# Kernel tuning notes

Measured on AMD Instinct MI355X. Metric: run time of the kernel, lower is better.

Reference implementation:

```python
import jax, jax.numpy as jnp
import numpy as np

L = 4        # transformer layers
C = 128      # width
CIN = 2      # obs channels
BS = 9       # boardsize
S = BS * BS  # attention sequence length (81)
EPS = 1e-5


def setup_inputs() -> dict:
    key = jax.random.key(0)
    ks = jax.random.split(key, 6)

    def w(k, shape, scale):
        return jax.random.normal(k, shape, dtype=jnp.float32) * scale

    return {
        "x": jax.random.normal(ks[0], (4, 32, BS, BS, CIN), dtype=jnp.float32),
        # input projection (stored as [in, out] so y = x @ W + b)
        "in_w": w(ks[1], (CIN, C), CIN ** -0.5),
        "in_b": jnp.zeros((C,), jnp.float32),
        # per-layer LayerNorm affine params
        "ln_g": jnp.ones((L, C), jnp.float32),
        "ln_b": jnp.zeros((L, C), jnp.float32),
        # per-layer qkv and output linears
        "qkv_w": w(ks[2], (L, C, 3 * C), C ** -0.5),
        "qkv_b": jnp.zeros((L, 3 * C), jnp.float32),
        "full_w": w(ks[3], (L, C, C), C ** -0.5),
        "full_b": jnp.zeros((L, C), jnp.float32),
        # final projection to 4 channels
        "out_w": w(ks[4], (C, 4), C ** -0.5),
        "out_b": jnp.zeros((4,), jnp.float32),
    }


def _layernorm(x, g, b):
    mu = jnp.mean(x, axis=-1, keepdims=True)
    var = jnp.var(x, axis=-1, keepdims=True)
    return (x - mu) * jax.lax.rsqrt(var + EPS) * g + b


def reference(x, in_w, in_b, ln_g, ln_b, qkv_w, qkv_b, full_w, full_b, out_w, out_b):
    T, B, H, W, _ = x.shape
    h = x @ in_w + in_b  # [T,B,H,W,C]
    for i in range(L):
        n = _layernorm(h.reshape(T * B, S, C), ln_g[i], ln_b[i])  # [TB,S,C]
        qkv = n @ qkv_w[i] + qkv_b[i]
        q, k, v = jnp.split(qkv, 3, axis=-1)  # each [TB,S,C]
        # per-channel attention: no reduction over C before softmax
        sim = jnp.einsum('bqc,bkc->bqkc', q, k)        # [TB,S,S,C]
        attn = jax.nn.softmax(sim, axis=2)             # softmax over k per channel
        att = jnp.einsum('bqkc,bkc->bqc', attn, v)     # [TB,S,C]
        att = att.reshape(T, B, H, W, C)
        y = jax.nn.relu(att @ full_w[i] + full_b[i])
        h = h + y
    return h @ out_w + out_b  # [T,B,H,W,4]
```

## Files before the change

kernel.cpp:

```cpp
#include <hip/hip_runtime.h>

#define NQKV_ 384
#define MAGIC_ 0x5CA1AB1E
#define HSTRIDE 140
#define QSTRIDE 65
#define KSTRIDE 66

typedef __bf16 bf;
typedef __attribute__((ext_vector_type(4))) __bf16 bf16x4;
typedef __attribute__((ext_vector_type(8))) __bf16 bf16x8;
typedef __attribute__((ext_vector_type(4))) float f32x4;

__device__ __forceinline__ float fast_exp2(float x) {
#if __has_builtin(__builtin_amdgcn_exp2f)
  return __builtin_amdgcn_exp2f(x);
#else
  return exp2f(x);
#endif
}
__device__ __forceinline__ float fast_rcp(float x) {
#if __has_builtin(__builtin_amdgcn_rcpf)
  return __builtin_amdgcn_rcpf(x);
#else
  return 1.0f / x;
#endif
}

__global__ __launch_bounds__(1024)
__attribute__((amdgpu_waves_per_eu(4, 4))) void k_net(
    const float* __restrict__ x, const float* __restrict__ in_w,
    const float* __restrict__ in_b, const float* __restrict__ ln_g,
    const float* __restrict__ ln_b, const float* __restrict__ qkv_w,
    const float* __restrict__ qkv_b, const float* __restrict__ full_w,
    const float* __restrict__ full_b, const float* __restrict__ out_w,
    const float* __restrict__ out_b, bf* __restrict__ wq,
    bf* __restrict__ wf, bf* __restrict__ attg,
    int* __restrict__ flags, int* __restrict__ pflags,
    float* __restrict__ out) {
  __shared__ __align__(16) float h_s[81 * HSTRIDE];
  __shared__ __align__(16) bf afrag[96 * 128];
  __shared__ float q_s[81 * QSTRIDE];
  __shared__ float kvf[81 * KSTRIDE * 2];

  const int tid = threadIdx.x;
  const int bidx = blockIdx.x;
  const int b = bidx & 127, half = bidx >> 7, c0 = half * 64;
  const int wave = tid >> 6, lane = tid & 63, l15 = lane & 15, quad = lane >> 4;
  const float log2e = 1.4426950408889634f;

  bf* ag_own = attg + (size_t)(b * 2 + half) * 6144;
  const bf* ag_peer = attg + (size_t)(b * 2 + (1 - half)) * 6144;

  {
    int p = bidx & 127, hp = bidx >> 7;
    int pl = p >> 5, u = p & 31;
    const float* srcw;
    bf* dstt;
    int ldn, n0;
    if (u < 24) {
      srcw = qkv_w + (size_t)pl * 128 * NQKV_;
      dstt = wq + ((size_t)(pl * 24 + u) << 11);
      ldn = NQKV_; n0 = u * 16;
    } else {
      srcw = full_w + (size_t)pl * 128 * 128;
      dstt = wf + ((size_t)(pl * 8 + (u - 24)) << 11);
      ldn = 128; n0 = (u - 24) * 16;
    }
    if (tid < 256) {
      int g = hp * 1024 + tid * 4;
      int s = g >> 9, l = (g >> 3) & 63, j0 = g & 7;
      int kb = s * 32 + ((l >> 4) << 3) + j0;
      int n = n0 + (l & 15);
      unsigned long long pk = 0;
#pragma unroll
      for (int jj = 0; jj < 4; ++jj) {
        bf v = (bf)srcw[(size_t)(kb + jj) * ldn + n];
        pk |= (unsigned long long)__builtin_bit_cast(unsigned short, v) << (16 * jj);
      }
      __hip_atomic_store((unsigned long long*)(dstt + g), pk, __ATOMIC_RELAXED,
                         __HIP_MEMORY_SCOPE_AGENT);
    }
    __syncthreads();
    if (tid == 0)
      __hip_atomic_store(&pflags[p * 2 + hp], MAGIC_, __ATOMIC_RELAXED,
                         __HIP_MEMORY_SCOPE_AGENT);
  }

  {
    const float* xb = x + (size_t)b * 162;
    for (int i = tid; i < 81 * 128; i += 1024) {
      int p = i >> 7, cc = i & 127;
      h_s[p * HSTRIDE + cc] = xb[p * 2] * in_w[cc] + xb[p * 2 + 1] * in_w[128 + cc] + in_b[cc];
    }
  }
  __syncthreads();

  for (int layer = 0; layer < 4; ++layer) {
    const bf* wqL = wq + (size_t)layer * 24 * 2048;
    const bf* wfL = wf + (size_t)layer * 8 * 2048;

    {
      const float* lg = ln_g + layer * 128;
      const float* lb = ln_b + layer * 128;
      int row = tid >> 3, g8 = tid & 7;
      if (row < 81) {
        const float* hr = h_s + row * HSTRIDE;
        float vals[16];
        float sum = 0.f, ssq = 0.f;
#pragma unroll
        for (int it = 0; it < 4; ++it) {
          float4 f = *(const float4*)(hr + g8 * 4 + it * 32);
          vals[it * 4 + 0] = f.x; vals[it * 4 + 1] = f.y;
          vals[it * 4 + 2] = f.z; vals[it * 4 + 3] = f.w;
          sum += f.x + f.y + f.z + f.w;
          ssq += f.x * f.x + f.y * f.y + f.z * f.z + f.w * f.w;
        }
#pragma unroll
        for (int off = 1; off < 8; off <<= 1) {
          sum += __shfl_xor(sum, off);
          ssq += __shfl_xor(ssq, off);
        }
        float mu = sum * (1.f / 128.f);
        float rs = rsqrtf(ssq * (1.f / 128.f) - mu * mu + 1e-5f);
        int mt = row >> 4, m = row & 15;
        int lgp = g8 >> 1, j0 = (g8 & 1) * 4;
#pragma unroll
        for (int it = 0; it < 4; ++it) {
          int cc = g8 * 4 + it * 32;
          float4 gg = *(const float4*)(lg + cc);
          float4 bb = *(const float4*)(lb + cc);
          bf16x4 nv;
          nv[0] = (bf)((vals[it * 4 + 0] - mu) * rs * gg.x + bb.x);
          nv[1] = (bf)((vals[it * 4 + 1] - mu) * rs * gg.y + bb.y);
          nv[2] = (bf)((vals[it * 4 + 2] - mu) * rs * gg.z + bb.z);
          nv[3] = (bf)((vals[it * 4 + 3] - mu) * rs * gg.w + bb.w);
          *(bf16x4*)(afrag + (((mt * 4 + it) * 64 + (lgp * 16 + m)) << 3) + j0) = nv;
        }
      }
    }
    __syncthreads();

    if (layer == 0) {
      if (wave == 0) {
        long guard = 0;
        for (;;) {
          int ok = 1;
#pragma unroll
          for (int t = 0; t < 4; ++t)
            ok &= (__hip_atomic_load(&pflags[t * 64 + lane], __ATOMIC_RELAXED,
                                     __HIP_MEMORY_SCOPE_AGENT) == MAGIC_);
          if (__all(ok)) break;
          __builtin_amdgcn_s_sleep(2);
          if (++guard > (1L << 24)) break;
        }
      }
      __syncthreads();
      __builtin_amdgcn_fence(__ATOMIC_ACQUIRE, "workgroup");
    }

    {
      f32x4 acc[5] = {};
#pragma unroll
      for (int i = 0; i < 5; ++i) {
        int tau = wave + 16 * i;
        if (tau < 72) {
          int Mt = tau / 12, Nt = tau % 12;
          int sec = Nt >> 2, off = Nt & 3;
          int tg = sec * 8 + half * 4 + off;
#pragma unroll
          for (int s = 0; s < 4; ++s) {
            bf16x8 a = *(const bf16x8*)(afrag + (((Mt * 4 + s) * 64 + lane) << 3));
            bf16x8 bb = *(const bf16x8*)(wqL + ((tg * 4 + s) * 512 + lane * 8));
            acc[i] = __builtin_amdgcn_mfma_f32_16x16x32_bf16(a, bb, acc[i], 0, 0, 0);
          }
        }
      }
      const float* qb = qkv_b + layer * NQKV_;
#pragma unroll
      for (int i = 0; i < 5; ++i) {
        int tau = wave + 16 * i;
        if (tau < 72) {
          int Mt = tau / 12, Nt = tau % 12;
          int sec = Nt >> 2, off = Nt & 3;
          int cl = off * 16 + l15;
          float bias = qb[sec * 128 + c0 + cl];
          int Rb = Mt * 16 + quad * 4;
#pragma unroll
          for (int r = 0; r < 4; ++r) {
            int R = Rb + r;
            if (R < 81) {
              float vv = acc[i][r] + bias;
              if (sec == 0)      q_s[R * QSTRIDE + cl] = vv * log2e;
              else if (sec == 1) kvf[(R * KSTRIDE + cl) * 2] = vv;
              else               kvf[(R * KSTRIDE + cl) * 2 + 1] = vv;
            }
          }
        }
      }
    }
    __syncthreads();

    {
      int c = tid & 63, qs = wave;
      int cc = c0 + c;
      unsigned int* agc = (unsigned int*)ag_own;
      unsigned int* afu = (unsigned int*)afrag;

      float xq[6], Na[6], Da[6];
#pragma unroll
      for (int j = 0; j < 5; ++j) {
        xq[j] = q_s[(qs + 16 * j) * QSTRIDE + c];
        Na[j] = 0.f; Da[j] = 0.f;
      }
      xq[5] = 0.f; Na[5] = 0.f; Da[5] = 0.f;
      if (qs == 0) {
        xq[5] = q_s[80 * QSTRIDE + c];
#pragma unroll 3
        for (int kk = 0; kk < 81; ++kk) {
          float2 A = *(const float2*)(kvf + (kk * KSTRIDE + c) * 2);
#pragma unroll
          for (int j = 0; j < 6; ++j) {
            float e = fast_exp2(xq[j] * A.x);
            Da[j] += e; Na[j] = __builtin_fmaf(e, A.y, Na[j]);
          }
        }
      } else {
#pragma unroll 3
        for (int kk = 0; kk < 81; ++kk) {
          float2 A = *(const float2*)(kvf + (kk * KSTRIDE + c) * 2);
#pragma unroll
          for (int j = 0; j < 5; ++j) {
            float e = fast_exp2(xq[j] * A.x);
            Da[j] += e; Na[j] = __builtin_fmaf(e, A.y, Na[j]);
          }
        }
      }
#pragma unroll
      for (int j = 0; j < 6; ++j) {
        if (j == 5 && qs != 0) break;
        int qq = qs + 16 * j;
        bf bv = (bf)(Na[j] * fast_rcp(Da[j]));
        unsigned int u = (unsigned int)__builtin_bit_cast(unsigned short, bv);
        unsigned int un = ((unsigned int)__shfl_xor((int)u, 1)) & 0xffffu;
        if ((c & 1) == 0) {
          unsigned int packed = u | (un << 16);
          int qc = (cc >> 3) & 3, jc = cc & 7, m = qq & 15, Mt = qq >> 4;
          int fragu = (((Mt * 4 + (cc >> 5)) * 512) + qc * 128 + m * 8 + jc) >> 1;
          afu[fragu] = packed;
          int compu = ((Mt * 1024) + ((cc >> 5) & 1) * 512 + qc * 128 + m * 8 + jc) >> 1;
          __hip_atomic_store(agc + compu, packed, __ATOMIC_RELAXED,
                             __HIP_MEMORY_SCOPE_AGENT);
        }
      }
    }
    __syncthreads();

    if (tid == 0) {
      __hip_atomic_store(&flags[bidx * 4 + layer], MAGIC_, __ATOMIC_RELAXED,
                         __HIP_MEMORY_SCOPE_AGENT);
    }
    f32x4 acc[3] = {};
    {
      int sbase = half * 2;
#pragma unroll
      for (int i = 0; i < 3; ++i) {
        int tau = wave + 16 * i;
        int Mt = tau >> 3, Nt = tau & 7;
#pragma unroll
        for (int ss = 0; ss < 2; ++ss) {
          int s = sbase + ss;
          bf16x8 a = *(const bf16x8*)(afrag + (((Mt * 4 + s) * 64 + lane) << 3));
          bf16x8 bb = *(const bf16x8*)(wfL + ((Nt * 4 + s) * 512 + lane * 8));
          acc[i] = __builtin_amdgcn_mfma_f32_16x16x32_bf16(a, bb, acc[i], 0, 0, 0);
        }
      }
    }
    if (tid == 0) {
      int peer = (bidx ^ 128) * 4 + layer;
      long guard = 0;
      while (__hip_atomic_load(&flags[peer], __ATOMIC_RELAXED,
                               __HIP_MEMORY_SCOPE_AGENT) != MAGIC_) {
        __builtin_amdgcn_s_sleep(2);
        if (++guard > (1L << 27)) break;
      }
    }
    __syncthreads();

    {
      const unsigned long long* peer8 = (const unsigned long long*)ag_peer;
      unsigned long long* af8 = (unsigned long long*)afrag;
      int sbaseG = 2 - half * 2;
      for (int t = tid; t < 1536; t += 1024) {
        int j = t & 1, ln2 = (t >> 1) & 63, ss = (t >> 7) & 1, Mt = t >> 8;
        unsigned long long v = __hip_atomic_load(peer8 + t, __ATOMIC_RELAXED,
                                                 __HIP_MEMORY_SCOPE_AGENT);
        af8[((Mt * 4 + sbaseG + ss) * 64 + ln2) * 2 + j] = v;
      }
    }
    __syncthreads();

    {
      int pbase = 2 - half * 2;
#pragma unroll
      for (int i = 0; i < 3; ++i) {
        int tau = wave + 16 * i;
        int Mt = tau >> 3, Nt = tau & 7;
#pragma unroll
        for (int ss = 0; ss < 2; ++ss) {
          int s = pbase + ss;
          bf16x8 a = *(const bf16x8*)(afrag + (((Mt * 4 + s) * 64 + lane) << 3));
          bf16x8 bb = *(const bf16x8*)(wfL + ((Nt * 4 + s) * 512 + lane * 8));
          acc[i] = __builtin_amdgcn_mfma_f32_16x16x32_bf16(a, bb, acc[i], 0, 0, 0);
        }
      }
      const float* fb = full_b + layer * 128;
#pragma unroll
      for (int i = 0; i < 3; ++i) {
        int tau = wave + 16 * i;
        int Mt = tau >> 3, Nt = tau & 7;
        int col = Nt * 16 + l15;
        float bias = fb[col];
        int Rb = Mt * 16 + quad * 4;
#pragma unroll
        for (int r = 0; r < 4; ++r) {
          int R = Rb + r;
          if (R < 81) h_s[R * HSTRIDE + col] += fmaxf(acc[i][r] + bias, 0.f);
        }
      }
    }
    __syncthreads();
  }

  if (half == 0) {
    int row = tid >> 3, g8 = tid & 7;
    if (row < 81) {
      const float* hr = h_s + row * HSTRIDE;
      float o0 = 0.f, o1 = 0.f, o2 = 0.f, o3 = 0.f;
#pragma unroll
      for (int it = 0; it < 4; ++it) {
        int cc = g8 * 4 + it * 32;
        float4 f = *(const float4*)(hr + cc);
        float4 wA = *(const float4*)(out_w + (cc + 0) * 4);
        float4 wB = *(const float4*)(out_w + (cc + 1) * 4);
        float4 wC = *(const float4*)(out_w + (cc + 2) * 4);
        float4 wD = *(const float4*)(out_w + (cc + 3) * 4);
        o0 += f.x * wA.x + f.y * wB.x + f.z * wC.x + f.w * wD.x;
        o1 += f.x * wA.y + f.y * wB.y + f.z * wC.y + f.w * wD.y;
        o2 += f.x * wA.z + f.y * wB.z + f.z * wC.z + f.w * wD.z;
        o3 += f.x * wA.w + f.y * wB.w + f.z * wC.w + f.w * wD.w;
      }
#pragma unroll
      for (int off = 1; off < 8; off <<= 1) {
        o0 += __shfl_xor(o0, off); o1 += __shfl_xor(o1, off);
        o2 += __shfl_xor(o2, off); o3 += __shfl_xor(o3, off);
      }
      if (g8 == 0) {
        *(float4*)(out + ((size_t)b * 81 + row) * 4) =
            make_float4(o0 + out_b[0], o1 + out_b[1], o2 + out_b[2], o3 + out_b[3]);
      }
    }
  }
}

extern "C" void kernel_launch(void* const* d_in, const int* in_sizes, int n_in,
                              void* d_out, int out_size, void* d_ws, size_t ws_size,
                              hipStream_t stream) {
  const float* x      = (const float*)d_in[0];
  const float* in_w   = (const float*)d_in[1];
  const float* in_b   = (const float*)d_in[2];
  const float* ln_g   = (const float*)d_in[3];
  const float* ln_b   = (const float*)d_in[4];
  const float* qkv_w  = (const float*)d_in[5];
  const float* qkv_b  = (const float*)d_in[6];
  const float* full_w = (const float*)d_in[7];
  const float* full_b = (const float*)d_in[8];
  const float* out_w  = (const float*)d_in[9];
  const float* out_b  = (const float*)d_in[10];

  bf* wq      = (bf*)d_ws;
  bf* wf      = wq + 196608;
  bf* attg    = wf + 65536;
  int* flags  = (int*)(attg + 1572864);
  int* pflags = flags + 1024;
  float* out  = (float*)d_out;

  k_net<<<256, 1024, 0, stream>>>(x, in_w, in_b, ln_g, ln_b, qkv_w, qkv_b,
                                  full_w, full_b, out_w, out_b, wq, wf, attg,
                                  flags, pflags, out);
}
```

Before: 177.3 us.

## Vectorize attention over channel pairs, repack K/V layout, and compact peer exchange

```diff
diff --git a/kernel.cpp b/kernel.cpp
--- a/kernel.cpp
+++ b/kernel.cpp
@@ -3,13 +3,14 @@
 #define NQKV_ 384
 #define MAGIC_ 0x5CA1AB1E
 #define HSTRIDE 140
-#define QSTRIDE 65
-#define KSTRIDE 66
+#define QSTRIDE 66
+#define KP 33
 
 typedef __bf16 bf;
 typedef __attribute__((ext_vector_type(4))) __bf16 bf16x4;
 typedef __attribute__((ext_vector_type(8))) __bf16 bf16x8;
 typedef __attribute__((ext_vector_type(4))) float f32x4;
+typedef __attribute__((ext_vector_type(2))) float f32x2;
 
 __device__ __forceinline__ float fast_exp2(float x) {
 #if __has_builtin(__builtin_amdgcn_exp2f)
@@ -39,8 +40,8 @@
     float* __restrict__ out) {
   __shared__ __align__(16) float h_s[81 * HSTRIDE];
   __shared__ __align__(16) bf afrag[96 * 128];
-  __shared__ float q_s[81 * QSTRIDE];
-  __shared__ float kvf[81 * KSTRIDE * 2];
+  __shared__ __align__(16) float q_s[81 * QSTRIDE];
+  __shared__ __align__(16) float kvf[81 * KP * 4];
 
   const int tid = threadIdx.x;
   const int bidx = blockIdx.x;
@@ -66,19 +67,25 @@
       dstt = wf + ((size_t)(pl * 8 + (u - 24)) << 11);
       ldn = 128; n0 = (u - 24) * 16;
     }
+    float (*tile)[17] = reinterpret_cast<float(*)[17]>(h_s);
     if (tid < 256) {
-      int g = hp * 1024 + tid * 4;
-      int s = g >> 9, l = (g >> 3) & 63, j0 = g & 7;
-      int kb = s * 32 + ((l >> 4) << 3) + j0;
-      int n = n0 + (l & 15);
+      int r = tid >> 2, c4 = (tid & 3) * 4;
+      float4 f = *(const float4*)(srcw + (size_t)(hp * 64 + r) * ldn + n0 + c4);
+      tile[r][c4 + 0] = f.x; tile[r][c4 + 1] = f.y;
+      tile[r][c4 + 2] = f.z; tile[r][c4 + 3] = f.w;
+    }
+    __syncthreads();
+    if (tid < 256) {
+      int s_loc = tid >> 7, l = (tid >> 1) & 63, j0 = (tid & 1) * 4;
+      int rbase = s_loc * 32 + ((l >> 4) << 3) + j0, col = l & 15;
       unsigned long long pk = 0;
 #pragma unroll
       for (int jj = 0; jj < 4; ++jj) {
-        bf v = (bf)srcw[(size_t)(kb + jj) * ldn + n];
+        bf v = (bf)tile[rbase + jj][col];
         pk |= (unsigned long long)__builtin_bit_cast(unsigned short, v) << (16 * jj);
       }
-      __hip_atomic_store((unsigned long long*)(dstt + g), pk, __ATOMIC_RELAXED,
-                         __HIP_MEMORY_SCOPE_AGENT);
+      __hip_atomic_store((unsigned long long*)(dstt + hp * 1024 + tid * 4), pk,
+                         __ATOMIC_RELAXED, __HIP_MEMORY_SCOPE_AGENT);
     }
     __syncthreads();
     if (tid == 0)
@@ -191,8 +198,8 @@
             if (R < 81) {
               float vv = acc[i][r] + bias;
               if (sec == 0)      q_s[R * QSTRIDE + cl] = vv * log2e;
-              else if (sec == 1) kvf[(R * KSTRIDE + cl) * 2] = vv;
-              else               kvf[(R * KSTRIDE + cl) * 2 + 1] = vv;
+              else if (sec == 1) kvf[(R * KP + (cl >> 1)) * 4 + (cl & 1)] = vv;
+              else               kvf[(R * KP + (cl >> 1)) * 4 + 2 + (cl & 1)] = vv;
             }
           }
         }
@@ -201,54 +208,45 @@
     __syncthreads();
 
     {
-      int c = tid & 63, qs = wave;
-      int cc = c0 + c;
+      int cp = tid & 31, qg = tid >> 5;
+      int nq = (qg <= 16) ? 3 : 2;
       unsigned int* agc = (unsigned int*)ag_own;
       unsigned int* afu = (unsigned int*)afrag;
 
-      float xq[6], Na[6], Da[6];
-#pragma unroll
-      for (int j = 0; j < 5; ++j) {
-        xq[j] = q_s[(qs + 16 * j) * QSTRIDE + c];
-        Na[j] = 0.f; Da[j] = 0.f;
-      }
-      xq[5] = 0.f; Na[5] = 0.f; Da[5] = 0.f;
-      if (qs == 0) {
-        xq[5] = q_s[80 * QSTRIDE + c];
+      f32x2 xq2[3] = {}, Na2[3] = {}, Da2[3] = {};
+#pragma unroll
+      for (int j = 0; j < 3; ++j)
+        if (j < nq) xq2[j] = *(const f32x2*)(q_s + (qg + 32 * j) * QSTRIDE + 2 * cp);
+
 #pragma unroll 3
-        for (int kk = 0; kk < 81; ++kk) {
-          float2 A = *(const float2*)(kvf + (kk * KSTRIDE + c) * 2);
-#pragma unroll
-          for (int j = 0; j < 6; ++j) {
-            float e = fast_exp2(xq[j] * A.x);
-            Da[j] += e; Na[j] = __builtin_fmaf(e, A.y, Na[j]);
+      for (int kk = 0; kk < 81; ++kk) {
+        float4 kv = *(const float4*)(kvf + (kk * KP + cp) * 4);
+        f32x2 k2 = {kv.x, kv.y}, v2 = {kv.z, kv.w};
+#pragma unroll
+        for (int j = 0; j < 3; ++j) {
+          if (j < nq) {
+            f32x2 arg = xq2[j] * k2;
+            f32x2 e;
+            e.x = fast_exp2(arg.x);
+            e.y = fast_exp2(arg.y);
+            Da2[j] += e;
+            Na2[j] += e * v2;
           }
         }
-      } else {
-#pragma unroll 3
-        for (int kk = 0; kk < 81; ++kk) {
-          float2 A = *(const float2*)(kvf + (kk * KSTRIDE + c) * 2);
-#pragma unroll
-          for (int j = 0; j < 5; ++j) {
-            float e = fast_exp2(xq[j] * A.x);
-            Da[j] += e; Na[j] = __builtin_fmaf(e, A.y, Na[j]);
-          }
-        }
-      }
-#pragma unroll
-      for (int j = 0; j < 6; ++j) {
-        if (j == 5 && qs != 0) break;
-        int qq = qs + 16 * j;
-        bf bv = (bf)(Na[j] * fast_rcp(Da[j]));
-        unsigned int u = (unsigned int)__builtin_bit_cast(unsigned short, bv);
-        unsigned int un = ((unsigned int)__shfl_xor((int)u, 1)) & 0xffffu;
-        if ((c & 1) == 0) {
-          unsigned int packed = u | (un << 16);
-          int qc = (cc >> 3) & 3, jc = cc & 7, m = qq & 15, Mt = qq >> 4;
-          int fragu = (((Mt * 4 + (cc >> 5)) * 512) + qc * 128 + m * 8 + jc) >> 1;
-          afu[fragu] = packed;
-          int compu = ((Mt * 1024) + ((cc >> 5) & 1) * 512 + qc * 128 + m * 8 + jc) >> 1;
-          __hip_atomic_store(agc + compu, packed, __ATOMIC_RELAXED,
+      }
+      int cc = c0 + 2 * cp;
+      int sc = cc >> 5, qc = (cc >> 3) & 3, jc = cc & 7;
+#pragma unroll
+      for (int j = 0; j < 3; ++j) {
+        if (j < nq) {
+          int qq = qg + 32 * j;
+          bf b0 = (bf)(Na2[j].x * fast_rcp(Da2[j].x));
+          bf b1 = (bf)(Na2[j].y * fast_rcp(Da2[j].y));
+          unsigned int packed = (unsigned int)__builtin_bit_cast(unsigned short, b0)
+                              | ((unsigned int)__builtin_bit_cast(unsigned short, b1) << 16);
+          int m = qq & 15, Mt = qq >> 4;
+          afu[(((Mt * 4 + sc) * 512) + qc * 128 + m * 8 + jc) >> 1] = packed;
+          __hip_atomic_store(agc + qq * 32 + cp, packed, __ATOMIC_RELAXED,
                              __HIP_MEMORY_SCOPE_AGENT);
         }
       }
@@ -289,12 +287,15 @@
     {
       const unsigned long long* peer8 = (const unsigned long long*)ag_peer;
       unsigned long long* af8 = (unsigned long long*)afrag;
-      int sbaseG = 2 - half * 2;
-      for (int t = tid; t < 1536; t += 1024) {
-        int j = t & 1, ln2 = (t >> 1) & 63, ss = (t >> 7) & 1, Mt = t >> 8;
+      int pc0 = 64 - c0;
+      for (int t = tid; t < 1296; t += 1024) {
+        int qq = t >> 4, cph = t & 15;
+        int cc = pc0 + cph * 4;
+        int sc = cc >> 5, qc = (cc >> 3) & 3, jc = cc & 7;
+        int m = qq & 15, Mt = qq >> 4;
         unsigned long long v = __hip_atomic_load(peer8 + t, __ATOMIC_RELAXED,
                                                  __HIP_MEMORY_SCOPE_AGENT);
-        af8[((Mt * 4 + sbaseG + ss) * 64 + ln2) * 2 + j] = v;
+        af8[(((Mt * 4 + sc) * 64 + qc * 16 + m) * 8 + jc) >> 2] = v;
       }
     }
     __syncthreads();
```

Measured after the change: 172.0 us. -3.0%, faster.
